# Kernel optimization log

Measured on AMD Instinct MI355X. Metric: run time of the kernel, lower is better.

The kernel has to match this reference:

```python
import jax, jax.numpy as jnp
import numpy as np

D = 768    # text_feature_dim (BERT)
H = 1024   # hidden_dim
L = 16384  # history length


def setup_inputs() -> dict:
    key = jax.random.key(0)
    ks = jax.random.split(key, 10)
    text_v = jax.random.normal(ks[0], (1, D), dtype=jnp.float32)
    result = jax.random.uniform(ks[1], (1,), dtype=jnp.float32)
    text_s = jax.random.normal(ks[2], (L, D), dtype=jnp.float32)
    hidden_s = jax.random.normal(ks[3], (L, H), dtype=jnp.float32)
    # GRU params (PyTorch layout: W_ih [3H, 2D], W_hh [3H, H]), uniform(-1/sqrt(H), 1/sqrt(H))
    s = 1.0 / np.sqrt(H)
    W_ih = jax.random.uniform(ks[4], (3 * H, 2 * D), minval=-s, maxval=s, dtype=jnp.float32)
    W_hh = jax.random.uniform(ks[5], (3 * H, H), minval=-s, maxval=s, dtype=jnp.float32)
    b_ih = jax.random.uniform(ks[6], (3 * H,), minval=-s, maxval=s, dtype=jnp.float32)
    b_hh = jax.random.uniform(ks[7], (3 * H,), minval=-s, maxval=s, dtype=jnp.float32)
    # score layer: Linear(D+H, 1)
    s2 = 1.0 / np.sqrt(D + H)
    score_W = jax.random.uniform(ks[8], (1, D + H), minval=-s2, maxval=s2, dtype=jnp.float32)
    score_b = jax.random.uniform(ks[9], (1,), minval=-s2, maxval=s2, dtype=jnp.float32)
    return {"text_v": text_v, "result": result, "text_s": text_s, "hidden_s": hidden_s,
            "W_ih": W_ih, "W_hh": W_hh, "b_ih": b_ih, "b_hh": b_hh,
            "score_W": score_W, "score_b": score_b}


def reference(text_v, result, text_s, hidden_s, W_ih, W_hh, b_ih, b_hh, score_W, score_b):
    # --- attention over growing history ---
    h = hidden_s[-1:, :]                                   # [1, H] last hidden state
    alpha = jax.nn.softmax(text_s @ text_v.T, axis=0)      # [L, 1]
    attn_h = alpha.T @ hidden_s                            # [1, H]

    # --- score prediction ---
    pred_v = jnp.concatenate([text_v, attn_h], axis=1)     # [1, D+H]
    score = pred_v @ score_W.T + score_b                   # [1, 1]

    # --- input gating by correctness ---
    zeros = jnp.zeros_like(text_v)
    x_r = jnp.where(result >= 0.5,
                    jnp.concatenate([text_v, zeros], axis=1),
                    jnp.concatenate([zeros, text_v], axis=1))  # [1, 2D]

    # --- GRU cell (PyTorch gate order: r, z, n) ---
    gi = x_r @ W_ih.T + b_ih                               # [1, 3H]
    gh = h @ W_hh.T + b_hh                                 # [1, 3H]
    i_r, i_z, i_n = jnp.split(gi, 3, axis=1)
    h_r, h_z, h_n = jnp.split(gh, 3, axis=1)
    r = jax.nn.sigmoid(i_r + h_r)
    z = jax.nn.sigmoid(i_z + h_z)
    n = jnp.tanh(i_n + r * h_n)
    h_new = (1.0 - z) * n + z * h                          # [1, H]

    return score[0], h_new                                 # score.squeeze(0) -> [1]
```

## Files before the change

kernel.cpp:

```cpp
#include <hip/hip_runtime.h>
#include <math.h>

#define LL 16384
#define Dm 768
#define Hm 1024

#define ATT_B 512
#define GI_B  192
#define GH_B  192
#define NP    2048
#define MID_B 64

#define WS_GI 0
#define WS_GH 3072
#define WS_PM 6144
#define WS_PS 8192
#define WS_PV 10240
#define WS_M2 (10240 + 2048*1024)
#define WS_S2 (WS_M2 + 64)
#define WS_V2 (WS_S2 + 64)

__device__ __forceinline__ float dot4(float4 a, float4 b) {
    return a.x*b.x + a.y*b.y + a.z*b.z + a.w*b.w;
}

__global__ __launch_bounds__(256) void k_main(
    const float* __restrict__ text_v, const float* __restrict__ result,
    const float* __restrict__ text_s, const float* __restrict__ hidden_s,
    const float* __restrict__ W_ih, const float* __restrict__ W_hh,
    const float* __restrict__ b_ih, const float* __restrict__ b_hh,
    float* __restrict__ ws)
{
    const int b    = blockIdx.x;
    const int tid  = threadIdx.x;
    const int lane = tid & 63;
    const int wv   = tid >> 6;

    if (b < ATT_B) {
        const int wid = b*4 + wv;
        const int r0  = wid*8;

        float4 tv0 = *(const float4*)(text_v + 4*lane);
        float4 tv1 = *(const float4*)(text_v + 4*lane + 256);
        float4 tv2 = *(const float4*)(text_v + 4*lane + 512);

        float4 x[8][3];
        #pragma unroll
        for (int i = 0; i < 8; ++i) {
            const float* p = text_s + (size_t)(r0 + i)*Dm + 4*lane;
            x[i][0] = *(const float4*)(p);
            x[i][1] = *(const float4*)(p + 256);
            x[i][2] = *(const float4*)(p + 512);
        }
        float pd[8];
        #pragma unroll
        for (int i = 0; i < 8; ++i)
            pd[i] = dot4(x[i][0], tv0) + dot4(x[i][1], tv1) + dot4(x[i][2], tv2);
        #pragma unroll
        for (int i = 0; i < 8; ++i) {
            #pragma unroll
            for (int o = 32; o; o >>= 1) pd[i] += __shfl_xor(pd[i], o);
        }

        float m = pd[0];
        #pragma unroll
        for (int i = 1; i < 8; ++i) m = fmaxf(m, pd[i]);
        float w[8], s = 0.f;
        #pragma unroll
        for (int i = 0; i < 8; ++i) { w[i] = expf(pd[i] - m); s += w[i]; }

        float4 acc[4] = {{0,0,0,0},{0,0,0,0},{0,0,0,0},{0,0,0,0}};
        #pragma unroll
        for (int c = 0; c < 2; ++c) {
            float4 hv[4][4];
            #pragma unroll
            for (int j = 0; j < 4; ++j) {
                const float* p = hidden_s + (size_t)(r0 + c*4 + j)*Hm + 4*lane;
                #pragma unroll
                for (int k = 0; k < 4; ++k) hv[j][k] = *(const float4*)(p + 256*k);
            }
            #pragma unroll
            for (int j = 0; j < 4; ++j) {
                const float wj = w[c*4 + j];
                #pragma unroll
                for (int k = 0; k < 4; ++k) {
                    acc[k].x += wj*hv[j][k].x; acc[k].y += wj*hv[j][k].y;
                    acc[k].z += wj*hv[j][k].z; acc[k].w += wj*hv[j][k].w;
                }
            }
        }
        #pragma unroll
        for (int k = 0; k < 4; ++k)
            *(float4*)(ws + WS_PV + (size_t)wid*1024 + 4*lane + 256*k) = acc[k];
        if (lane == 0) {
            ws[WS_PM + wid] = m;
            ws[WS_PS + wid] = s;
        }
    } else if (b < ATT_B + GI_B) {
        const int gb  = b - ATT_B;
        const int off = (result[0] >= 0.5f) ? 0 : Dm;
        float4 tv0 = *(const float4*)(text_v + 4*lane);
        float4 tv1 = *(const float4*)(text_v + 4*lane + 256);
        float4 tv2 = *(const float4*)(text_v + 4*lane + 512);
        const int kbase = gb*16 + wv*4;
        float4 x[4][3];
        #pragma unroll
        for (int i = 0; i < 4; ++i) {
            const float* p = W_ih + (size_t)(kbase + i)*(2*Dm) + off + 4*lane;
            x[i][0] = *(const float4*)(p);
            x[i][1] = *(const float4*)(p + 256);
            x[i][2] = *(const float4*)(p + 512);
        }
        #pragma unroll
        for (int i = 0; i < 4; ++i) {
            float s = dot4(x[i][0], tv0) + dot4(x[i][1], tv1) + dot4(x[i][2], tv2);
            #pragma unroll
            for (int o = 32; o; o >>= 1) s += __shfl_xor(s, o);
            const int k = kbase + i;
            if (lane == 0) ws[WS_GI + k] = s + b_ih[k];
        }
    } else {
        const int hb = b - ATT_B - GI_B;
        const float* h = hidden_s + (size_t)(LL - 1)*Hm;
        float4 h0 = *(const float4*)(h + 4*lane);
        float4 h1 = *(const float4*)(h + 4*lane + 256);
        float4 h2 = *(const float4*)(h + 4*lane + 512);
        float4 h3 = *(const float4*)(h + 4*lane + 768);
        const int kbase = hb*16 + wv*4;
        float4 x[4][4];
        #pragma unroll
        for (int i = 0; i < 4; ++i) {
            const float* p = W_hh + (size_t)(kbase + i)*Hm + 4*lane;
            x[i][0] = *(const float4*)(p);
            x[i][1] = *(const float4*)(p + 256);
            x[i][2] = *(const float4*)(p + 512);
            x[i][3] = *(const float4*)(p + 768);
        }
        #pragma unroll
        for (int i = 0; i < 4; ++i) {
            float s = dot4(x[i][0], h0) + dot4(x[i][1], h1)
                    + dot4(x[i][2], h2) + dot4(x[i][3], h3);
            #pragma unroll
            for (int o = 32; o; o >>= 1) s += __shfl_xor(s, o);
            const int k = kbase + i;
            if (lane == 0) ws[WS_GH + k] = s + b_hh[k];
        }
    }
}

__global__ __launch_bounds__(256) void k_mid(float* __restrict__ ws) {
    __shared__ float sm[32];
    __shared__ float sc[32];
    const int b  = blockIdx.x;
    const int t  = threadIdx.x;
    const int p0 = b * 32;
    if (t < 32) sm[t] = ws[WS_PM + p0 + t];
    __syncthreads();
    float m = sm[0];
    #pragma unroll
    for (int r = 1; r < 32; ++r) m = fmaxf(m, sm[r]);
    if (t < 32) sc[t] = expf(sm[t] - m);
    __syncthreads();

    float4 acc = {0.f, 0.f, 0.f, 0.f};
    #pragma unroll
    for (int c = 0; c < 4; ++c) {
        float4 hv[8];
        #pragma unroll
        for (int r = 0; r < 8; ++r)
            hv[r] = *(const float4*)(ws + WS_PV + (size_t)(p0 + c*8 + r)*1024 + 4*t);
        #pragma unroll
        for (int r = 0; r < 8; ++r) {
            const float w = sc[c*8 + r];
            acc.x += w*hv[r].x; acc.y += w*hv[r].y;
            acc.z += w*hv[r].z; acc.w += w*hv[r].w;
        }
    }
    *(float4*)(ws + WS_V2 + (size_t)b*1024 + 4*t) = acc;
    if (t == 0) {
        float s = 0.f;
        #pragma unroll
        for (int r = 0; r < 32; ++r) s += sc[r] * ws[WS_PS + p0 + r];
        ws[WS_M2 + b] = m;
        ws[WS_S2 + b] = s;
    }
}

__global__ __launch_bounds__(1024) void k_final(
    const float* __restrict__ text_v, const float* __restrict__ hidden_s,
    const float* __restrict__ score_W, const float* __restrict__ score_b,
    float* __restrict__ ws, float* __restrict__ out)
{
    __shared__ float sred[16];
    const int tid = threadIdx.x;
    float mbuf[8], M;
    #pragma unroll
    for (int i = 0; i < 8; ++i) mbuf[i] = ws[WS_M2 + i*8];
    M = ws[WS_M2];
    #pragma unroll
    for (int r = 1; r < 64; ++r) M = fmaxf(M, ws[WS_M2 + r]);
    (void)mbuf;
    float S = 0.f, a = 0.f;
    #pragma unroll
    for (int c = 0; c < 8; ++c) {
        float scl[8], vv[8];
        #pragma unroll
        for (int r = 0; r < 8; ++r) {
            scl[r] = expf(ws[WS_M2 + c*8 + r] - M);
            vv[r]  = ws[WS_V2 + (c*8 + r)*1024 + tid];
        }
        #pragma unroll
        for (int r = 0; r < 8; ++r) {
            S += scl[r] * ws[WS_S2 + c*8 + r];
            a += scl[r] * vv[r];
        }
    }
    a /= S;
    float sp = a * score_W[Dm + tid];
    if (tid < Dm) sp += text_v[tid] * score_W[tid];
    #pragma unroll
    for (int o = 32; o; o >>= 1) sp += __shfl_xor(sp, o);
    if ((tid & 63) == 0) sred[tid >> 6] = sp;
    __syncthreads();
    if (tid == 0) {
        float s = score_b[0];
        #pragma unroll
        for (int i = 0; i < 16; ++i) s += sred[i];
        out[0] = s;
    }
    const float gi_r = ws[WS_GI + tid];
    const float gi_z = ws[WS_GI + 1024 + tid];
    const float gi_n = ws[WS_GI + 2048 + tid];
    const float gh_r = ws[WS_GH + tid];
    const float gh_z = ws[WS_GH + 1024 + tid];
    const float gh_n = ws[WS_GH + 2048 + tid];
    const float hprev = hidden_s[(size_t)(LL - 1)*Hm + tid];
    const float r = 1.f / (1.f + expf(-(gi_r + gh_r)));
    const float z = 1.f / (1.f + expf(-(gi_z + gh_z)));
    const float n = tanhf(gi_n + r*gh_n);
    out[1 + tid] = (1.f - z)*n + z*hprev;
}

extern "C" void kernel_launch(void* const* d_in, const int* in_sizes, int n_in,
                              void* d_out, int out_size, void* d_ws, size_t ws_size,
                              hipStream_t stream) {
    const float* text_v   = (const float*)d_in[0];
    const float* result   = (const float*)d_in[1];
    const float* text_s   = (const float*)d_in[2];
    const float* hidden_s = (const float*)d_in[3];
    const float* W_ih     = (const float*)d_in[4];
    const float* W_hh     = (const float*)d_in[5];
    const float* b_ih     = (const float*)d_in[6];
    const float* b_hh     = (const float*)d_in[7];
    const float* score_W  = (const float*)d_in[8];
    const float* score_b  = (const float*)d_in[9];
    float* out = (float*)d_out;
    float* ws  = (float*)d_ws;

    k_main <<<ATT_B + GI_B + GH_B, 256, 0, stream>>>(
        text_v, result, text_s, hidden_s, W_ih, W_hh, b_ih, b_hh, ws);
    k_mid  <<<MID_B, 256, 0, stream>>>(ws);
    k_final<<<1, 1024, 0, stream>>>(text_v, hidden_s, score_W, score_b, ws, out);
}
```

Baseline: 193.6 us.

## Combine wave partials in shared memory to halve attention partial workspace

Attention blocks now handle 16 rows (4 per wave) across twice as many blocks. Each block merges its four wave-level softmax partials in LDS before writing one 1024-float partial, so the intermediate partial-vector traffic through global memory is halved. The middle reduction stage uses half as many blocks and the final kernel reads 32 partials instead of 64. Register use per wave is lower, with launch bounds raised for occupancy, at the cost of one __syncthreads and LDS use per attention block.

```diff
diff --git a/kernel.cpp b/kernel.cpp
--- a/kernel.cpp
+++ b/kernel.cpp
@@ -5,26 +5,25 @@
 #define Dm 768
 #define Hm 1024
 
-#define ATT_B 512
+#define ATT_B 1024
 #define GI_B  192
 #define GH_B  192
-#define NP    2048
-#define MID_B 64
+#define MID_B 32
 
 #define WS_GI 0
 #define WS_GH 3072
 #define WS_PM 6144
-#define WS_PS 8192
-#define WS_PV 10240
-#define WS_M2 (10240 + 2048*1024)
-#define WS_S2 (WS_M2 + 64)
-#define WS_V2 (WS_S2 + 64)
+#define WS_PS 7168
+#define WS_PV 8192
+#define WS_M2 (8192 + 1024*1024)
+#define WS_S2 (WS_M2 + 32)
+#define WS_V2 (WS_S2 + 32)
 
 __device__ __forceinline__ float dot4(float4 a, float4 b) {
     return a.x*b.x + a.y*b.y + a.z*b.z + a.w*b.w;
 }
 
-__global__ __launch_bounds__(256) void k_main(
+__global__ __launch_bounds__(256, 4) void k_main(
     const float* __restrict__ text_v, const float* __restrict__ result,
     const float* __restrict__ text_s, const float* __restrict__ hidden_s,
     const float* __restrict__ W_ih, const float* __restrict__ W_hh,
@@ -37,64 +36,90 @@
     const int wv   = tid >> 6;
 
     if (b < ATT_B) {
-        const int wid = b*4 + wv;
-        const int r0  = wid*8;
+        __shared__ float sacc[4][1024];
+        __shared__ float smx[4], ssm[4];
+        const int r0 = b*16 + wv*4;
 
         float4 tv0 = *(const float4*)(text_v + 4*lane);
         float4 tv1 = *(const float4*)(text_v + 4*lane + 256);
         float4 tv2 = *(const float4*)(text_v + 4*lane + 512);
 
-        float4 x[8][3];
-        #pragma unroll
-        for (int i = 0; i < 8; ++i) {
+        float4 x[4][3];
+        #pragma unroll
+        for (int i = 0; i < 4; ++i) {
             const float* p = text_s + (size_t)(r0 + i)*Dm + 4*lane;
             x[i][0] = *(const float4*)(p);
             x[i][1] = *(const float4*)(p + 256);
             x[i][2] = *(const float4*)(p + 512);
         }
-        float pd[8];
-        #pragma unroll
-        for (int i = 0; i < 8; ++i)
+        float4 hv0[2][4];
+        #pragma unroll
+        for (int j = 0; j < 2; ++j) {
+            const float* p = hidden_s + (size_t)(r0 + j)*Hm + 4*lane;
+            #pragma unroll
+            for (int k = 0; k < 4; ++k) hv0[j][k] = *(const float4*)(p + 256*k);
+        }
+
+        float pd[4];
+        #pragma unroll
+        for (int i = 0; i < 4; ++i)
             pd[i] = dot4(x[i][0], tv0) + dot4(x[i][1], tv1) + dot4(x[i][2], tv2);
         #pragma unroll
-        for (int i = 0; i < 8; ++i) {
+        for (int i = 0; i < 4; ++i) {
             #pragma unroll
             for (int o = 32; o; o >>= 1) pd[i] += __shfl_xor(pd[i], o);
         }
 
-        float m = pd[0];
-        #pragma unroll
-        for (int i = 1; i < 8; ++i) m = fmaxf(m, pd[i]);
-        float w[8], s = 0.f;
-        #pragma unroll
-        for (int i = 0; i < 8; ++i) { w[i] = expf(pd[i] - m); s += w[i]; }
-
-        float4 acc[4] = {{0,0,0,0},{0,0,0,0},{0,0,0,0},{0,0,0,0}};
-        #pragma unroll
-        for (int c = 0; c < 2; ++c) {
-            float4 hv[4][4];
-            #pragma unroll
-            for (int j = 0; j < 4; ++j) {
-                const float* p = hidden_s + (size_t)(r0 + c*4 + j)*Hm + 4*lane;
-                #pragma unroll
-                for (int k = 0; k < 4; ++k) hv[j][k] = *(const float4*)(p + 256*k);
-            }
-            #pragma unroll
-            for (int j = 0; j < 4; ++j) {
-                const float wj = w[c*4 + j];
-                #pragma unroll
-                for (int k = 0; k < 4; ++k) {
-                    acc[k].x += wj*hv[j][k].x; acc[k].y += wj*hv[j][k].y;
-                    acc[k].z += wj*hv[j][k].z; acc[k].w += wj*hv[j][k].w;
-                }
-            }
-        }
+        float m = fmaxf(fmaxf(pd[0], pd[1]), fmaxf(pd[2], pd[3]));
+        float w[4], s = 0.f;
+        #pragma unroll
+        for (int i = 0; i < 4; ++i) { w[i] = expf(pd[i] - m); s += w[i]; }
+
+        float4 hv1[2][4];
+        #pragma unroll
+        for (int j = 0; j < 2; ++j) {
+            const float* p = hidden_s + (size_t)(r0 + 2 + j)*Hm + 4*lane;
+            #pragma unroll
+            for (int k = 0; k < 4; ++k) hv1[j][k] = *(const float4*)(p + 256*k);
+        }
+        float4 acc[4];
+        #pragma unroll
+        for (int k = 0; k < 4; ++k) {
+            acc[k].x = w[0]*hv0[0][k].x + w[1]*hv0[1][k].x;
+            acc[k].y = w[0]*hv0[0][k].y + w[1]*hv0[1][k].y;
+            acc[k].z = w[0]*hv0[0][k].z + w[1]*hv0[1][k].z;
+            acc[k].w = w[0]*hv0[0][k].w + w[1]*hv0[1][k].w;
+        }
+        #pragma unroll
+        for (int k = 0; k < 4; ++k) {
+            acc[k].x += w[2]*hv1[0][k].x + w[3]*hv1[1][k].x;
+            acc[k].y += w[2]*hv1[0][k].y + w[3]*hv1[1][k].y;
+            acc[k].z += w[2]*hv1[0][k].z + w[3]*hv1[1][k].z;
+            acc[k].w += w[2]*hv1[0][k].w + w[3]*hv1[1][k].w;
+        }
+
         #pragma unroll
         for (int k = 0; k < 4; ++k)
-            *(float4*)(ws + WS_PV + (size_t)wid*1024 + 4*lane + 256*k) = acc[k];
-        if (lane == 0) {
-            ws[WS_PM + wid] = m;
-            ws[WS_PS + wid] = s;
+            *(float4*)&sacc[wv][4*lane + 256*k] = acc[k];
+        if (lane == 0) { smx[wv] = m; ssm[wv] = s; }
+        __syncthreads();
+
+        const float M = fmaxf(fmaxf(smx[0], smx[1]), fmaxf(smx[2], smx[3]));
+        float sc0 = expf(smx[0] - M), sc1 = expf(smx[1] - M);
+        float sc2 = expf(smx[2] - M), sc3 = expf(smx[3] - M);
+        float4 v0 = *(const float4*)&sacc[0][4*tid];
+        float4 v1 = *(const float4*)&sacc[1][4*tid];
+        float4 v2 = *(const float4*)&sacc[2][4*tid];
+        float4 v3 = *(const float4*)&sacc[3][4*tid];
+        float4 r;
+        r.x = sc0*v0.x + sc1*v1.x + sc2*v2.x + sc3*v3.x;
+        r.y = sc0*v0.y + sc1*v1.y + sc2*v2.y + sc3*v3.y;
+        r.z = sc0*v0.z + sc1*v1.z + sc2*v2.z + sc3*v3.z;
+        r.w = sc0*v0.w + sc1*v1.w + sc2*v2.w + sc3*v3.w;
+        *(float4*)(ws + WS_PV + (size_t)b*1024 + 4*tid) = r;
+        if (tid == 0) {
+            ws[WS_PM + b] = M;
+            ws[WS_PS + b] = sc0*ssm[0] + sc1*ssm[1] + sc2*ssm[2] + sc3*ssm[3];
         }
     } else if (b < ATT_B + GI_B) {
         const int gb  = b - ATT_B;
@@ -193,16 +218,12 @@
 {
     __shared__ float sred[16];
     const int tid = threadIdx.x;
-    float mbuf[8], M;
-    #pragma unroll
-    for (int i = 0; i < 8; ++i) mbuf[i] = ws[WS_M2 + i*8];
-    M = ws[WS_M2];
-    #pragma unroll
-    for (int r = 1; r < 64; ++r) M = fmaxf(M, ws[WS_M2 + r]);
-    (void)mbuf;
+    float M = ws[WS_M2];
+    #pragma unroll
+    for (int r = 1; r < 32; ++r) M = fmaxf(M, ws[WS_M2 + r]);
     float S = 0.f, a = 0.f;
     #pragma unroll
-    for (int c = 0; c < 8; ++c) {
+    for (int c = 0; c < 4; ++c) {
         float scl[8], vv[8];
         #pragma unroll
         for (int r = 0; r < 8; ++r) {
```

Measured after the change: 188.8 us. 1.03x faster.
